# Optimization experiments

Measured on AMD Instinct MI355X. Metric: run time of the kernel, lower is better.

Reference implementation:

```python
import jax, jax.numpy as jnp
import numpy as np

D_MODEL = 1024
N_HEADS = 16
HEAD_DIM = D_MODEL // N_HEADS


def setup_inputs() -> dict:
    key = jax.random.key(0)
    k_x, k_w1, k_b1, k_w2, k_b2 = jax.random.split(key, 5)
    B, S = 4, 2048
    x = jax.random.normal(k_x, (B, S, D_MODEL), dtype=jnp.float32)
    # torch Linear init ~ U(-1/sqrt(fan_in), 1/sqrt(fan_in))
    lim = 1.0 / np.sqrt(D_MODEL)
    qkv_w = jax.random.uniform(k_w1, (D_MODEL, 3 * D_MODEL), jnp.float32, -lim, lim)
    qkv_b = jax.random.uniform(k_b1, (3 * D_MODEL,), jnp.float32, -lim, lim)
    out_w = jax.random.uniform(k_w2, (D_MODEL, D_MODEL), jnp.float32, -lim, lim)
    out_b = jax.random.uniform(k_b2, (D_MODEL,), jnp.float32, -lim, lim)
    return {"x": x, "qkv_w": qkv_w, "qkv_b": qkv_b, "out_w": out_w, "out_b": out_b}


def reference(x, qkv_w, qkv_b, out_w, out_b):
    B, S, D = x.shape
    scale = HEAD_DIM ** -0.5
    qkv = x @ qkv_w + qkv_b  # [B,S,3D]
    q, k, v = jnp.split(qkv, 3, axis=-1)
    def to_heads(t):
        return t.reshape(B, S, N_HEADS, HEAD_DIM).transpose(0, 2, 1, 3)  # [B,H,S,Dh]
    q, k, v = to_heads(q), to_heads(k), to_heads(v)
    scores = jnp.einsum('bhqd,bhkd->bhqk', q, k) * scale  # [B,H,S,S]
    causal = jnp.tril(jnp.ones((S, S), dtype=bool))
    scores = jnp.where(causal, scores, -jnp.inf)
    weights = jax.nn.softmax(scores, axis=-1)  # dropout is identity in eval
    out = jnp.einsum('bhqk,bhkd->bhqd', weights, v)  # [B,H,S,Dh]
    out = out.transpose(0, 2, 1, 3).reshape(B, S, D)
    return out @ out_w + out_b
```

## Files before the change

### kernel.cpp

```cpp
#include <hip/hip_runtime.h>

typedef __bf16 bf16x8 __attribute__((ext_vector_type(8)));
typedef float f32x4 __attribute__((ext_vector_type(4)));
typedef unsigned short u16;

#define D_MODEL 1024
#define SEQ     2048
#define BATCH   4
#define NH      16
#define DH      64

static __device__ __forceinline__ u16 f2bf(float f) {
    union { float f; unsigned u; } v; v.f = f;
    unsigned r = v.u + 0x7FFF + ((v.u >> 16) & 1);
    return (u16)(r >> 16);
}
static __device__ __forceinline__ void storeC(u16* C, size_t off, float v) { C[off] = f2bf(v); }
static __device__ __forceinline__ void storeC(float* C, size_t off, float v) { C[off] = v; }

static __device__ __forceinline__ void async_ld16(u16* lds, const u16* g) {
    __builtin_amdgcn_global_load_lds(
        (const __attribute__((address_space(1))) unsigned int*)g,
        (__attribute__((address_space(3))) unsigned int*)lds, 16, 0, 0);
}

__global__ __launch_bounds__(256) void cvt_bf16(const float* __restrict__ in,
                                                u16* __restrict__ out) {
    size_t i = ((size_t)blockIdx.x * 256 + threadIdx.x) * 8;
    float4 a = *(const float4*)(in + i);
    float4 b = *(const float4*)(in + i + 4);
    u16 t[8] = {f2bf(a.x), f2bf(a.y), f2bf(a.z), f2bf(a.w),
                f2bf(b.x), f2bf(b.y), f2bf(b.z), f2bf(b.w)};
    *(uint4*)(out + i) = *(uint4*)t;
}

__global__ void transpose_w(const float* __restrict__ in, u16* __restrict__ out,
                            int K, int N) {
    __shared__ float tile[32][33];
    int n0 = blockIdx.x * 32, k0 = blockIdx.y * 32;
    int tx = threadIdx.x, ty = threadIdx.y;
    for (int i = ty; i < 32; i += 8)
        tile[i][tx] = in[(size_t)(k0 + i) * N + n0 + tx];
    __syncthreads();
    for (int i = ty; i < 32; i += 8)
        out[(size_t)(n0 + i) * K + k0 + tx] = f2bf(tile[tx][i]);
}

template <typename CT>
__global__ __launch_bounds__(256) void gemm_bt(
    const u16* __restrict__ A, int lda,
    const u16* __restrict__ Bt, int ldb,
    const float* __restrict__ bias,
    CT* __restrict__ C, int ldc, int K) {
    __shared__ u16 As[128 * 64];
    __shared__ u16 Bs[128 * 64];
    int m0 = blockIdx.x * 128, n0 = blockIdx.y * 128;
    int tid = threadIdx.x;
    int w = tid >> 6, lane = tid & 63, l15 = lane & 15, g = lane >> 4;
    int wm = (w & 1) * 64, wn = (w >> 1) * 64;
    int srow = w * 8 + (lane >> 3);
    int sk8  = lane & 7;

    f32x4 acc[4][4] = {};
    for (int kt = 0; kt < K; kt += 64) {
        #pragma unroll
        for (int p = 0; p < 4; ++p) {
            int row = p * 32 + srow;
            int k8 = sk8 ^ (row & 7);
            async_ld16(&As[p * 2048 + w * 512],
                       A + (size_t)(m0 + row) * lda + kt + k8 * 8);
            async_ld16(&Bs[p * 2048 + w * 512],
                       Bt + (size_t)(n0 + row) * ldb + kt + k8 * 8);
        }
        __syncthreads();
        #pragma unroll
        for (int kk = 0; kk < 2; ++kk) {
            bf16x8 af[4], bf_[4];
            int s8 = ((kk << 2) | g) ^ (l15 & 7);
            #pragma unroll
            for (int i = 0; i < 4; ++i) {
                af[i]  = *(const bf16x8*)&As[(wm + i * 16 + l15) * 64 + s8 * 8];
                bf_[i] = *(const bf16x8*)&Bs[(wn + i * 16 + l15) * 64 + s8 * 8];
            }
            #pragma unroll
            for (int i = 0; i < 4; ++i)
                #pragma unroll
                for (int j = 0; j < 4; ++j)
                    acc[i][j] = __builtin_amdgcn_mfma_f32_16x16x32_bf16(
                        af[i], bf_[j], acc[i][j], 0, 0, 0);
        }
        __syncthreads();
    }
    #pragma unroll
    for (int j = 0; j < 4; ++j) {
        int n = n0 + wn + j * 16 + l15;
        float bv = bias[n];
        #pragma unroll
        for (int i = 0; i < 4; ++i) {
            int mbase = m0 + wm + i * 16 + g * 4;
            #pragma unroll
            for (int r = 0; r < 4; ++r)
                storeC(C, (size_t)(mbase + r) * ldc + n, acc[i][j][r] + bv);
        }
    }
}

__global__ __launch_bounds__(256) void gemm_qkv(
    const u16* __restrict__ A,
    const u16* __restrict__ Bt,
    const float* __restrict__ bias,
    u16* __restrict__ Qd, u16* __restrict__ pkK, u16* __restrict__ pkV) {
    __shared__ u16 As[128 * 64];
    __shared__ u16 Bs[128 * 64];
    const int K = D_MODEL;
    int m0 = blockIdx.x * 128, n0 = blockIdx.y * 128;
    int tid = threadIdx.x;
    int w = tid >> 6, lane = tid & 63, l15 = lane & 15, g = lane >> 4;
    int wm = (w & 1) * 64, wn = (w >> 1) * 64;
    int srow = w * 8 + (lane >> 3);
    int sk8  = lane & 7;

    f32x4 acc[4][4] = {};
    for (int kt = 0; kt < K; kt += 64) {
        #pragma unroll
        for (int p = 0; p < 4; ++p) {
            int row = p * 32 + srow;
            int k8 = sk8 ^ (row & 7);
            async_ld16(&As[p * 2048 + w * 512],
                       A + (size_t)(m0 + row) * K + kt + k8 * 8);
            async_ld16(&Bs[p * 2048 + w * 512],
                       Bt + (size_t)(n0 + row) * K + kt + k8 * 8);
        }
        __syncthreads();
        #pragma unroll
        for (int kk = 0; kk < 2; ++kk) {
            bf16x8 af[4], bf_[4];
            int s8 = ((kk << 2) | g) ^ (l15 & 7);
            #pragma unroll
            for (int i = 0; i < 4; ++i) {
                af[i]  = *(const bf16x8*)&As[(wm + i * 16 + l15) * 64 + s8 * 8];
                bf_[i] = *(const bf16x8*)&Bs[(wn + i * 16 + l15) * 64 + s8 * 8];
            }
            #pragma unroll
            for (int i = 0; i < 4; ++i)
                #pragma unroll
                for (int j = 0; j < 4; ++j)
                    acc[i][j] = __builtin_amdgcn_mfma_f32_16x16x32_bf16(
                        af[i], bf_[j], acc[i][j], 0, 0, 0);
        }
        __syncthreads();
    }
    #pragma unroll
    for (int j = 0; j < 4; ++j) {
        int n = n0 + wn + j * 16 + l15;
        float bv = bias[n];
        int region = n >> 10;
        int hd = n & 1023;
        int h = hd >> 6, d = hd & 63;
        #pragma unroll
        for (int i = 0; i < 4; ++i) {
            #pragma unroll
            for (int r = 0; r < 4; ++r) {
                int m = m0 + wm + i * 16 + g * 4 + r;
                u16 vb = f2bf(acc[i][j][r] + bv);
                int b = m >> 11, s = m & 2047;
                int t = s >> 6, kap = s & 63;
                if (region == 0) {
                    Qd[(size_t)m * 1024 + hd] = vb;
                } else if (region == 1) {
                    int bh = b * 16 + h;
                    int nb = kap >> 4, lk = kap & 15;
                    int kk = d >> 5, gk = (d >> 3) & 3, jk = d & 7;
                    pkK[(size_t)(bh * 32 + t) * 4096 +
                        ((nb * 2 + kk) * 64 + gk * 16 + lk) * 8 + jk] = vb;
                } else {
                    int bh = b * 16 + h;
                    int kk = kap >> 5, gv = (kap >> 3) & 3, jv = kap & 7;
                    int nb = d >> 4, lv = d & 15;
                    pkV[(size_t)(bh * 32 + t) * 4096 +
                        ((nb * 2 + kk) * 64 + gv * 16 + lv) * 8 + jv] = vb;
                }
            }
        }
    }
}

__global__ __launch_bounds__(256) void attn_flash(
    u16* __restrict__ Qd, const u16* __restrict__ pkK,
    const u16* __restrict__ pkV) {
    __shared__ __align__(16) char smemraw[18432 + 256];
    u16 (*Pt)[32][72] = (u16(*)[32][72])smemraw;
    float* Om = (float*)smemraw;
    float* Lm = (float*)(smemraw + 18432);

    int bh = blockIdx.x, b = bh >> 4, h = bh & 15;
    int tid = threadIdx.x;
    int w = tid >> 6, lane = tid & 63, l15 = lane & 15, g = lane >> 4;
    int wq = w >> 1, wk = w & 1;

    const u16* Kb = pkK + (size_t)bh * 32 * 4096;
    const u16* Vb = pkV + (size_t)bh * 32 * 4096;
    u16* Qbase = Qd + (size_t)b * SEQ * 1024 + h * DH;

    int qts[2] = {31 - (int)blockIdx.y, (int)blockIdx.y};

    #pragma unroll
    for (int qi = 0; qi < 2; ++qi) {
        int qt = qts[qi];
        int q0 = qt * 64;

        bf16x8 qfrag[2][2];
        #pragma unroll
        for (int st = 0; st < 2; ++st) {
            const u16* qp = Qbase + (size_t)(q0 + wq * 32 + st * 16 + l15) * 1024 + g * 8;
            bf16x8 a = *(const bf16x8*)qp;
            bf16x8 c = *(const bf16x8*)(qp + 32);
            #pragma unroll
            for (int jj = 0; jj < 8; ++jj) {
                a[jj] = (__bf16)((float)a[jj] * 0.125f);
                c[jj] = (__bf16)((float)c[jj] * 0.125f);
            }
            qfrag[st][0] = a; qfrag[st][1] = c;
        }

        f32x4 o[2][4] = {};
        float lsum[2][4] = {};

        for (int t = wk; t <= qt; t += 2) {
            const u16* kt = Kb + t * 4096;
            const u16* vt = Vb + t * 4096;
            bf16x8 kf[4][2], vf[4][2];
            #pragma unroll
            for (int nb = 0; nb < 4; ++nb) {
                #pragma unroll
                for (int kk = 0; kk < 2; ++kk) {
                    kf[nb][kk] = *(const bf16x8*)(kt + ((nb * 2 + kk) * 64 + lane) * 8);
                    vf[nb][kk] = *(const bf16x8*)(vt + ((nb * 2 + kk) * 64 + lane) * 8);
                }
            }
            bool diag = (t == qt);
            int k0 = t * 64;

            #pragma unroll
            for (int st = 0; st < 2; ++st) {
                f32x4 s[4] = {};
                #pragma unroll
                for (int nb = 0; nb < 4; ++nb)
                    #pragma unroll
                    for (int kk = 0; kk < 2; ++kk)
                        s[nb] = __builtin_amdgcn_mfma_f32_16x16x32_bf16(
                            qfrag[st][kk], kf[nb][kk], s[nb], 0, 0, 0);

                #pragma unroll
                for (int r = 0; r < 4; ++r) {
                    int qg = q0 + wq * 32 + st * 16 + g * 4 + r;
                    #pragma unroll
                    for (int nb = 0; nb < 4; ++nb) {
                        float p = __expf(s[nb][r]);
                        if (diag && (k0 + nb * 16 + l15) > qg) p = 0.f;
                        lsum[st][r] += p;
                        Pt[w][st * 16 + g * 4 + r][nb * 16 + l15] =
                            (u16)(__float_as_uint(p) >> 16);
                    }
                }

                #pragma unroll
                for (int kk = 0; kk < 2; ++kk) {
                    bf16x8 aP = *(const bf16x8*)&Pt[w][st * 16 + l15][kk * 32 + g * 8];
                    #pragma unroll
                    for (int nb = 0; nb < 4; ++nb)
                        o[st][nb] = __builtin_amdgcn_mfma_f32_16x16x32_bf16(
                            aP, vf[nb][kk], o[st][nb], 0, 0, 0);
                }
            }
        }

        #pragma unroll
        for (int msk = 1; msk < 16; msk <<= 1)
            #pragma unroll
            for (int st = 0; st < 2; ++st)
                #pragma unroll
                for (int r = 0; r < 4; ++r)
                    lsum[st][r] += __shfl_xor(lsum[st][r], msk, 64);

        __syncthreads();
        if (wk == 0) {
            #pragma unroll
            for (int st = 0; st < 2; ++st)
                #pragma unroll
                for (int r = 0; r < 4; ++r) {
                    int qrow = wq * 32 + st * 16 + g * 4 + r;
                    if (l15 == 0) Lm[qrow] = lsum[st][r];
                    #pragma unroll
                    for (int nb = 0; nb < 4; ++nb)
                        Om[qrow * 65 + nb * 16 + l15] = o[st][nb][r];
                }
        }
        __syncthreads();
        if (wk == 1) {
            #pragma unroll
            for (int st = 0; st < 2; ++st)
                #pragma unroll
                for (int r = 0; r < 4; ++r) {
                    int qrow = wq * 32 + st * 16 + g * 4 + r;
                    float inv = 1.f / (lsum[st][r] + Lm[qrow]);
                    u16* op = Qbase + (size_t)(q0 + qrow) * 1024;
                    #pragma unroll
                    for (int nb = 0; nb < 4; ++nb) {
                        float val = (o[st][nb][r] + Om[qrow * 65 + nb * 16 + l15]) * inv;
                        op[nb * 16 + l15] = f2bf(val);
                    }
                }
        }
        __syncthreads();
    }
}

extern "C" void kernel_launch(void* const* d_in, const int* in_sizes, int n_in,
                              void* d_out, int out_size, void* d_ws, size_t ws_size,
                              hipStream_t stream) {
    const float* x     = (const float*)d_in[0];
    const float* qkv_w = (const float*)d_in[1];
    const float* qkv_b = (const float*)d_in[2];
    const float* out_w = (const float*)d_in[3];
    const float* out_b = (const float*)d_in[4];
    float* out = (float*)d_out;

    const int M = BATCH * SEQ;
    u16* Qd     = (u16*)d_ws;
    u16* pkK    = Qd  + (size_t)M * D_MODEL;
    u16* pkV    = pkK + (size_t)64 * 32 * 4096;
    u16* xb     = pkV + (size_t)64 * 32 * 4096;
    u16* Wqkv_t = xb  + (size_t)M * D_MODEL;
    u16* Wout_t = Wqkv_t + (size_t)3 * D_MODEL * D_MODEL;

    cvt_bf16<<<(size_t)M * D_MODEL / (256 * 8), 256, 0, stream>>>(x, xb);
    transpose_w<<<dim3(3 * D_MODEL / 32, D_MODEL / 32), dim3(32, 8), 0, stream>>>(
        qkv_w, Wqkv_t, D_MODEL, 3 * D_MODEL);
    transpose_w<<<dim3(D_MODEL / 32, D_MODEL / 32), dim3(32, 8), 0, stream>>>(
        out_w, Wout_t, D_MODEL, D_MODEL);

    gemm_qkv<<<dim3(M / 128, 3 * D_MODEL / 128), 256, 0, stream>>>(
        xb, Wqkv_t, qkv_b, Qd, pkK, pkV);

    attn_flash<<<dim3(BATCH * NH, SEQ / 64 / 2), 256, 0, stream>>>(Qd, pkK, pkV);

    gemm_bt<float><<<dim3(M / 128, D_MODEL / 128), 256, 0, stream>>>(
        Qd, D_MODEL, Wout_t, D_MODEL, out_b, out, D_MODEL, D_MODEL);
}
```

Baseline: 272.5 us.

## Restructure QKV GEMM into 256x256 double-buffered pipelined tiles with block swizzle

```diff
diff --git a/kernel.cpp b/kernel.cpp
--- a/kernel.cpp
+++ b/kernel.cpp
@@ -105,51 +105,108 @@
     }
 }
 
-__global__ __launch_bounds__(256) void gemm_qkv(
+__global__ __launch_bounds__(512, 2) void gemm_qkv(
     const u16* __restrict__ A,
     const u16* __restrict__ Bt,
     const float* __restrict__ bias,
     u16* __restrict__ Qd, u16* __restrict__ pkK, u16* __restrict__ pkV) {
-    __shared__ u16 As[128 * 64];
-    __shared__ u16 Bs[128 * 64];
+    __shared__ u16 As[2][16384];
+    __shared__ u16 Bs[2][16384];
     const int K = D_MODEL;
-    int m0 = blockIdx.x * 128, n0 = blockIdx.y * 128;
+
+    int lid = blockIdx.x;
+    int swz = (lid & 7) * 48 + (lid >> 3);
+    int m0 = (swz & 31) * 256;
+    int n0 = (swz >> 5) * 256;
+
     int tid = threadIdx.x;
     int w = tid >> 6, lane = tid & 63, l15 = lane & 15, g = lane >> 4;
-    int wm = (w & 1) * 64, wn = (w >> 1) * 64;
-    int srow = w * 8 + (lane >> 3);
-    int sk8  = lane & 7;
-
-    f32x4 acc[4][4] = {};
+    int wm = (w >> 2) * 128, wn = (w & 3) * 64;
+    int srow = tid >> 3, sg = tid & 7;
+
+    const u16* Ab = A + (size_t)m0 * K;
+    const u16* Bb = Bt + (size_t)n0 * K;
+
+    auto stageA = [&](int buf, int c, int kt) {
+        int row = c * 64 + srow;
+        int k8 = sg ^ (row & 7);
+        async_ld16(&As[buf][(c * 64 + w * 8) * 64],
+                   Ab + (size_t)row * K + kt + k8 * 8);
+    };
+    auto stageB = [&](int buf, int c, int kt) {
+        int row = c * 64 + srow;
+        int k8 = sg ^ (row & 7);
+        async_ld16(&Bs[buf][(c * 64 + w * 8) * 64],
+                   Bb + (size_t)row * K + kt + k8 * 8);
+    };
+    auto rdA = [&](int cur, int i, int kk) {
+        return *(const bf16x8*)&As[cur][(wm + i * 16 + l15) * 64 +
+                                        ((((kk << 2) | g) ^ (l15 & 7)) * 8)];
+    };
+    auto rdB = [&](int cur, int j, int kk) {
+        return *(const bf16x8*)&Bs[cur][(wn + j * 16 + l15) * 64 +
+                                        ((((kk << 2) | g) ^ (l15 & 7)) * 8)];
+    };
+
+    f32x4 acc[8][4] = {};
+
+    stageB(0, 0, 0); stageB(0, 1, 0); stageB(0, 2, 0); stageB(0, 3, 0);
+    stageA(0, 0, 0); stageA(0, 2, 0); stageA(0, 1, 0); stageA(0, 3, 0);
+    asm volatile("s_waitcnt vmcnt(2)" ::: "memory");
+    __builtin_amdgcn_s_barrier();
+
+#define PHASE(i0, STAGE_STMT, ENDWAIT_STMT)                                      \
+    do {                                                                         \
+        bf16x8 a00 = rdA(cur, (i0), 0), a01 = rdA(cur, (i0), 1);                 \
+        bf16x8 a10 = rdA(cur, (i0) + 1, 0), a11 = rdA(cur, (i0) + 1, 1);         \
+        STAGE_STMT;                                                              \
+        __builtin_amdgcn_s_barrier();                                            \
+        asm volatile("s_waitcnt lgkmcnt(0)" ::: "memory");                       \
+        __builtin_amdgcn_s_setprio(1);                                           \
+        _Pragma("unroll")                                                        \
+        for (int j = 0; j < 4; ++j) {                                            \
+            acc[(i0)][j] = __builtin_amdgcn_mfma_f32_16x16x32_bf16(              \
+                a00, bfr[j][0], acc[(i0)][j], 0, 0, 0);                          \
+            acc[(i0)][j] = __builtin_amdgcn_mfma_f32_16x16x32_bf16(              \
+                a01, bfr[j][1], acc[(i0)][j], 0, 0, 0);                          \
+            acc[(i0) + 1][j] = __builtin_amdgcn_mfma_f32_16x16x32_bf16(          \
+                a10, bfr[j][0], acc[(i0) + 1][j], 0, 0, 0);                      \
+            acc[(i0) + 1][j] = __builtin_amdgcn_mfma_f32_16x16x32_bf16(          \
+                a11, bfr[j][1], acc[(i0) + 1][j], 0, 0, 0);                      \
+        }                                                                        \
+        __builtin_amdgcn_s_setprio(0);                                           \
+        ENDWAIT_STMT;                                                            \
+        __builtin_amdgcn_s_barrier();                                            \
+    } while (0)
+
     for (int kt = 0; kt < K; kt += 64) {
-        #pragma unroll
-        for (int p = 0; p < 4; ++p) {
-            int row = p * 32 + srow;
-            int k8 = sk8 ^ (row & 7);
-            async_ld16(&As[p * 2048 + w * 512],
-                       A + (size_t)(m0 + row) * K + kt + k8 * 8);
-            async_ld16(&Bs[p * 2048 + w * 512],
-                       Bt + (size_t)(n0 + row) * K + kt + k8 * 8);
-        }
-        __syncthreads();
-        #pragma unroll
-        for (int kk = 0; kk < 2; ++kk) {
-            bf16x8 af[4], bf_[4];
-            int s8 = ((kk << 2) | g) ^ (l15 & 7);
-            #pragma unroll
-            for (int i = 0; i < 4; ++i) {
-                af[i]  = *(const bf16x8*)&As[(wm + i * 16 + l15) * 64 + s8 * 8];
-                bf_[i] = *(const bf16x8*)&Bs[(wn + i * 16 + l15) * 64 + s8 * 8];
-            }
-            #pragma unroll
-            for (int i = 0; i < 4; ++i)
-                #pragma unroll
-                for (int j = 0; j < 4; ++j)
-                    acc[i][j] = __builtin_amdgcn_mfma_f32_16x16x32_bf16(
-                        af[i], bf_[j], acc[i][j], 0, 0, 0);
-        }
-        __syncthreads();
+        int cur = (kt >> 6) & 1, nxt = cur ^ 1;
+        int ktn = kt + 64;
+        bool hn = ktn < K;
+
+        bf16x8 bfr[4][2];
+        #pragma unroll
+        for (int j = 0; j < 4; ++j)
+            #pragma unroll
+            for (int kk = 0; kk < 2; ++kk)
+                bfr[j][kk] = rdB(cur, j, kk);
+
+        PHASE(0,
+              if (hn) { stageB(nxt, 0, ktn); stageB(nxt, 1, ktn); },
+              );
+        PHASE(2,
+              if (hn) { stageB(nxt, 2, ktn); stageB(nxt, 3, ktn); },
+              if (hn) { asm volatile("s_waitcnt vmcnt(4)" ::: "memory"); }
+              else    { asm volatile("s_waitcnt vmcnt(0)" ::: "memory"); });
+        PHASE(4,
+              if (hn) { stageA(nxt, 0, ktn); stageA(nxt, 2, ktn); },
+              );
+        PHASE(6,
+              if (hn) { stageA(nxt, 1, ktn); stageA(nxt, 3, ktn); },
+              asm volatile("s_waitcnt vmcnt(2)" ::: "memory"); );
     }
+#undef PHASE
+
     #pragma unroll
     for (int j = 0; j < 4; ++j) {
         int n = n0 + wn + j * 16 + l15;
@@ -158,7 +215,7 @@
         int hd = n & 1023;
         int h = hd >> 6, d = hd & 63;
         #pragma unroll
-        for (int i = 0; i < 4; ++i) {
+        for (int i = 0; i < 8; ++i) {
             #pragma unroll
             for (int r = 0; r < 4; ++r) {
                 int m = m0 + wm + i * 16 + g * 4 + r;
@@ -340,8 +397,7 @@
     transpose_w<<<dim3(D_MODEL / 32, D_MODEL / 32), dim3(32, 8), 0, stream>>>(
         out_w, Wout_t, D_MODEL, D_MODEL);
 
-    gemm_qkv<<<dim3(M / 128, 3 * D_MODEL / 128), 256, 0, stream>>>(
-        xb, Wqkv_t, qkv_b, Qd, pkK, pkV);
+    gemm_qkv<<<dim3(384), 512, 0, stream>>>(xb, Wqkv_t, qkv_b, Qd, pkK, pkV);
 
     attn_flash<<<dim3(BATCH * NH, SEQ / 64 / 2), 256, 0, stream>>>(Qd, pkK, pkV);
 
```

Result: no change. 277.8 us (+1.9%).

## Double-buffer LDS tiles in QKV and output GEMMs to overlap loads

Applied to the files above, without the earlier changes.

```diff
diff --git a/kernel.cpp b/kernel.cpp
--- a/kernel.cpp
+++ b/kernel.cpp
@@ -52,8 +52,8 @@
     const u16* __restrict__ Bt, int ldb,
     const float* __restrict__ bias,
     CT* __restrict__ C, int ldc, int K) {
-    __shared__ u16 As[128 * 64];
-    __shared__ u16 Bs[128 * 64];
+    __shared__ u16 As[2][128 * 64];
+    __shared__ u16 Bs[2][128 * 64];
     int m0 = blockIdx.x * 128, n0 = blockIdx.y * 128;
     int tid = threadIdx.x;
     int w = tid >> 6, lane = tid & 63, l15 = lane & 15, g = lane >> 4;
@@ -61,26 +61,33 @@
     int srow = w * 8 + (lane >> 3);
     int sk8  = lane & 7;
 
-    f32x4 acc[4][4] = {};
-    for (int kt = 0; kt < K; kt += 64) {
+    auto stage = [&](int buf, int kt) {
         #pragma unroll
         for (int p = 0; p < 4; ++p) {
             int row = p * 32 + srow;
             int k8 = sk8 ^ (row & 7);
-            async_ld16(&As[p * 2048 + w * 512],
+            async_ld16(&As[buf][p * 2048 + w * 512],
                        A + (size_t)(m0 + row) * lda + kt + k8 * 8);
-            async_ld16(&Bs[p * 2048 + w * 512],
+            async_ld16(&Bs[buf][p * 2048 + w * 512],
                        Bt + (size_t)(n0 + row) * ldb + kt + k8 * 8);
         }
-        __syncthreads();
+    };
+
+    f32x4 acc[4][4] = {};
+
+    stage(0, 0);
+    __syncthreads();
+    for (int kt = 0; kt < K; kt += 64) {
+        int cur = (kt >> 6) & 1;
+        if (kt + 64 < K) stage(cur ^ 1, kt + 64);
         #pragma unroll
         for (int kk = 0; kk < 2; ++kk) {
             bf16x8 af[4], bf_[4];
             int s8 = ((kk << 2) | g) ^ (l15 & 7);
             #pragma unroll
             for (int i = 0; i < 4; ++i) {
-                af[i]  = *(const bf16x8*)&As[(wm + i * 16 + l15) * 64 + s8 * 8];
-                bf_[i] = *(const bf16x8*)&Bs[(wn + i * 16 + l15) * 64 + s8 * 8];
+                af[i]  = *(const bf16x8*)&As[cur][(wm + i * 16 + l15) * 64 + s8 * 8];
+                bf_[i] = *(const bf16x8*)&Bs[cur][(wn + i * 16 + l15) * 64 + s8 * 8];
             }
             #pragma unroll
             for (int i = 0; i < 4; ++i)
@@ -110,8 +117,8 @@
     const u16* __restrict__ Bt,
     const float* __restrict__ bias,
     u16* __restrict__ Qd, u16* __restrict__ pkK, u16* __restrict__ pkV) {
-    __shared__ u16 As[128 * 64];
-    __shared__ u16 Bs[128 * 64];
+    __shared__ u16 As[2][128 * 64];
+    __shared__ u16 Bs[2][128 * 64];
     const int K = D_MODEL;
     int m0 = blockIdx.x * 128, n0 = blockIdx.y * 128;
     int tid = threadIdx.x;
@@ -120,26 +127,33 @@
     int srow = w * 8 + (lane >> 3);
     int sk8  = lane & 7;
 
-    f32x4 acc[4][4] = {};
-    for (int kt = 0; kt < K; kt += 64) {
+    auto stage = [&](int buf, int kt) {
         #pragma unroll
         for (int p = 0; p < 4; ++p) {
             int row = p * 32 + srow;
             int k8 = sk8 ^ (row & 7);
-            async_ld16(&As[p * 2048 + w * 512],
+            async_ld16(&As[buf][p * 2048 + w * 512],
                        A + (size_t)(m0 + row) * K + kt + k8 * 8);
-            async_ld16(&Bs[p * 2048 + w * 512],
+            async_ld16(&Bs[buf][p * 2048 + w * 512],
                        Bt + (size_t)(n0 + row) * K + kt + k8 * 8);
         }
-        __syncthreads();
+    };
+
+    f32x4 acc[4][4] = {};
+
+    stage(0, 0);
+    __syncthreads();
+    for (int kt = 0; kt < K; kt += 64) {
+        int cur = (kt >> 6) & 1;
+        if (kt + 64 < K) stage(cur ^ 1, kt + 64);
         #pragma unroll
         for (int kk = 0; kk < 2; ++kk) {
             bf16x8 af[4], bf_[4];
             int s8 = ((kk << 2) | g) ^ (l15 & 7);
             #pragma unroll
             for (int i = 0; i < 4; ++i) {
-                af[i]  = *(const bf16x8*)&As[(wm + i * 16 + l15) * 64 + s8 * 8];
-                bf_[i] = *(const bf16x8*)&Bs[(wn + i * 16 + l15) * 64 + s8 * 8];
+                af[i]  = *(const bf16x8*)&As[cur][(wm + i * 16 + l15) * 64 + s8 * 8];
+                bf_[i] = *(const bf16x8*)&Bs[cur][(wn + i * 16 + l15) * 64 + s8 * 8];
             }
             #pragma unroll
             for (int i = 0; i < 4; ++i)
```

After: 255.9 us. -6.1%, faster.
